# Performance work log

Measured on AMD Instinct MI355X. Metric: run time of the kernel, lower is better.

## Reference

```python
import jax, jax.numpy as jnp
import numpy as np

V = 100000   # num_node (item vocab)
D = 256      # config.dim
B = 512      # sessions / target nodes
S = 20       # items per session
N = B * S    # item nodes
E = 8 * N    # 'interacts' edges
SCALE = 12.0
NEG = -jnp.inf


def l2norm(x, eps=1e-12):
    return x / jnp.maximum(jnp.linalg.norm(x, axis=-1, keepdims=True), eps)


def setup_inputs() -> dict:
    key = jax.random.key(0)
    ks = jax.random.split(key, 16)
    stdv = 1.0 / np.sqrt(D)
    u = lambda k, shape: jax.random.uniform(k, shape, jnp.float32, -stdv, stdv)
    iid = jax.random.randint(ks[0], (N,), 0, V)
    src = jax.random.randint(ks[1], (E,), 0, N)
    # keep interacts edges within the same session (faithful to session graphs)
    dst = (src // S) * S + jax.random.randint(ks[2], (E,), 0, S)
    dis = jax.random.randint(ks[3], (E,), 0, 50)
    agg_src = jnp.arange(N)          # every item node -> its session target
    agg_dst = agg_src // S           # target (session) id per agg edge
    pid = agg_src % S                # position within session
    tid = jax.random.randint(ks[4], (B,), 0, 10)
    last_idx = jnp.arange(B) * S + (S - 1)   # nodes with data['last']==1
    return {
        'iid': iid, 'src': src, 'dst': dst, 'dis': dis, 'pid': pid,
        'agg_src': agg_src, 'agg_dst': agg_dst, 'tid': tid, 'last_idx': last_idx,
        'emb': u(ks[5], (V, D)), 'pos_emb': u(ks[6], (200, D)),
        'dis_emb': u(ks[7], (50, D)), 'target_emb': u(ks[8], (10, D)),
        'pi_w': u(ks[9], (D, 1)), 'M_w': u(ks[10], (2 * D, 1)),
        'q_w': u(ks[11], (2 * D, D)), 'r_w': u(ks[12], (2 * D, D)),
        'sc1_w': u(ks[13], (D, D)), 'sc1_b': u(ks[14], (D,)),
        'sc2_w': u(ks[15], (D, 2)),
    }


def reference(iid, src, dst, dis, pid, agg_src, agg_dst, tid, last_idx,
              emb, pos_emb, dis_emb, target_emb, pi_w, M_w, q_w, r_w,
              sc1_w, sc1_b, sc2_w):
    # --- node/edge features (dropout = identity at eval) ---
    h_v = l2norm(emb[iid])                       # [N,D]
    h_d = dis_emb[dis]                           # [E,D]
    # --- GATLayer on 'interacts' ---
    hs, hd = h_v[src], h_v[dst]
    prod = hs * hd                               # [E,D]
    e = (prod * h_d) @ pi_w                      # [E,1]
    gate = jax.nn.sigmoid(jnp.concatenate([prod, h_d], axis=-1) @ M_w)
    e = (e * gate)[:, 0]                         # [E]
    # edge_softmax grouped by destination node
    emax = jax.ops.segment_max(e, dst, num_segments=N)
    ee = jnp.exp(e - emax[dst])
    esum = jax.ops.segment_sum(ee, dst, num_segments=N)
    a = ee / esum[dst]                           # [E]
    h = jax.ops.segment_sum(hs * a[:, None], dst, num_segments=N)  # [N,D]
    # --- PosAggregator on 'agg' ---
    h_p = pos_emb[pid]                           # [EA,D]
    h_t = target_emb[tid]                        # [B,D]
    eft = h[agg_src]                             # copy_src ft -> edge ft
    eagg = jnp.tanh(jnp.concatenate([eft, h_p], axis=-1) @ q_w)    # [EA,D]
    last_feat = h[last_idx]                      # [B,D]
    f = jnp.concatenate([h_t, last_feat], axis=-1) @ r_w           # [B,D]
    m = eft * jnp.sum(eagg * f[agg_dst], axis=-1, keepdims=True)
    sr = jax.ops.segment_sum(m, agg_dst, num_segments=B)           # [B,D]
    # --- scoring head ---
    sr = l2norm(sr)
    bn = l2norm(emb)
    logits = sr @ bn.T                           # [B,V]
    phi = jax.nn.softmax(jax.nn.relu(sr @ sc1_w + sc1_b) @ sc2_w, axis=-1)  # [B,2]
    sess = jnp.arange(N) // S                    # session id of each item node
    mask = jnp.zeros((B, V), bool).at[sess, iid].set(True)
    score_in = jax.nn.softmax(jnp.where(mask, SCALE * logits, NEG), axis=-1)
    score_ex = jax.nn.softmax(jnp.where(mask, NEG, SCALE * logits), axis=-1)
    score = phi[:, 0:1] * score_in + phi[:, 1:2] * score_ex
    return jnp.log(score)
```

## Files before the change

kernel.cpp:

```cpp
#include <hip/hip_runtime.h>

typedef unsigned short u16;
typedef unsigned int u32;

constexpr int N_ = 10240, E_ = 81920, B_ = 512, S_ = 20, V_ = 100000, D_ = 256;
constexpr float SCALE_ = 12.0f;

#define DEV static __device__ __forceinline__

typedef __attribute__((ext_vector_type(8))) short bf16x8;
typedef __attribute__((ext_vector_type(4))) float f32x4;

DEV float bf2f(u16 u){ union{u32 i; float f;} c; c.i = ((u32)u)<<16; return c.f; }
DEV float bflo(u32 u){ union{u32 i; float f;} c; c.i = u<<16; return c.f; }
DEV float bfhi(u32 u){ union{u32 i; float f;} c; c.i = u & 0xffff0000u; return c.f; }
DEV u16 f2bf(float f){ union{float f; u32 i;} c; c.f=f; u32 i=c.i; i += 0x7fffu + ((i>>16)&1u); return (u16)(i>>16); }
DEV float clampf(float x, float lo, float hi){ return fminf(fmaxf(x, lo), hi); }

DEV float ldf(const void* p, size_t idx, int isf32){
  return isf32 ? ((const float*)p)[idx] : bf2f(((const u16*)p)[idx]);
}
DEV float rdout(const void* p, size_t idx, int isf32){
  return isf32 ? ((const float*)p)[idx] : bf2f(((const u16*)p)[idx]);
}
DEV void stout(void* p, size_t idx, float v, int isf32){
  if (isf32) ((float*)p)[idx] = v; else ((u16*)p)[idx] = f2bf(v);
}

DEV float waveSum(float v){
  #pragma unroll
  for (int off=32; off>0; off>>=1) v += __shfl_xor(v, off, 64);
  return v;
}
DEV float blockSum(float v, float* sred){
  v = waveSum(v);
  __syncthreads();
  if ((threadIdx.x & 63)==0) sred[threadIdx.x>>6] = v;
  __syncthreads();
  return sred[0]+sred[1]+sred[2]+sred[3];
}

__global__ __launch_bounds__(128) void k_detect(
    const u32* p0, const u32* p1, const u32* p2, const u32* p3,
    const u32* p4, const u32* p5, const u32* p6, const u32* p7,
    const u32* p8, const u32* p9, const u32* p10, int* flags)
{
  const u32* p = p0;
  switch (blockIdx.x){
    case 0: p=p0; break; case 1: p=p1; break; case 2: p=p2; break; case 3: p=p3; break;
    case 4: p=p4; break; case 5: p=p5; break; case 6: p=p6; break; case 7: p=p7; break;
    case 8: p=p8; break; case 9: p=p9; break; case 10: p=p10; break;
  }
  int t = threadIdx.x;
  u32 w = p[t];
  u32 e = (w>>8)&0x7Fu;
  int in = (e>=0x60u && e<=0x7Cu) ? 1 : 0;
  unsigned long long m = __ballot(in);
  __shared__ int cnt2[2];
  if ((t&63)==0) cnt2[t>>6] = __popcll(m);
  __syncthreads();
  if (t==0) flags[blockIdx.x] = ((cnt2[0]+cnt2[1]) > 96) ? 0 : 1;
}


__global__ __launch_bounds__(256) void k_splitB(const void* __restrict__ emb,
    u16* __restrict__ ehi, u16* __restrict__ elo, const int* __restrict__ flags)
{
  if (!flags[0]) return;
  size_t i = ((size_t)blockIdx.x*256 + threadIdx.x)*4;
  float4 x = *(const float4*)((const float*)emb + i);
  ushort4 h, l;
  h.x = f2bf(x.x); l.x = f2bf(x.x - bf2f(h.x));
  h.y = f2bf(x.y); l.y = f2bf(x.y - bf2f(h.y));
  h.z = f2bf(x.z); l.z = f2bf(x.z - bf2f(h.z));
  h.w = f2bf(x.w); l.w = f2bf(x.w - bf2f(h.w));
  *(ushort4*)(ehi+i) = h;
  *(ushort4*)(elo+i) = l;
}

__global__ __launch_bounds__(256) void k_rnorm(const void* __restrict__ emb,
    float* __restrict__ rnorm, const int* __restrict__ flags)
{
  int isf32 = flags[0];
  int v = blockIdx.x*4 + (threadIdx.x>>6);
  int lane = threadIdx.x & 63;
  float a0,a1,a2,a3;
  if (isf32){
    float4 q = *(const float4*)((const float*)emb + (size_t)v*D_ + lane*4);
    a0=q.x; a1=q.y; a2=q.z; a3=q.w;
  } else {
    uint2 p = *(const uint2*)((const u16*)emb + (size_t)v*D_ + lane*4);
    a0=bflo(p.x); a1=bfhi(p.x); a2=bflo(p.y); a3=bfhi(p.y);
  }
  float ss = waveSum(a0*a0+a1*a1+a2*a2+a3*a3);
  if (lane==0) rnorm[v] = 1.0f/fmaxf(sqrtf(ss), 1e-12f);
}

__global__ __launch_bounds__(256) void k_edge(
    const void* __restrict__ emb, const void* __restrict__ dis_emb,
    const void* __restrict__ pi_w, const void* __restrict__ M_w,
    const int* __restrict__ iid, const float* __restrict__ rnorm,
    const int* __restrict__ src, const int* __restrict__ dst, const int* __restrict__ dis,
    float* __restrict__ e_edge, const int* __restrict__ flags)
{
  int f_emb = flags[0], f_dis = flags[2], f_pi = flags[4], f_M = flags[5];
  int e = blockIdx.x*4 + (threadIdx.x>>6);
  int lane = threadIdx.x & 63;
  int s = src[e], d = dst[e], di = dis[e];
  int is = iid[s], idd = iid[d];
  float rs = rnorm[is], rd = rnorm[idd];
  int k0 = lane*4;
  float d1 = 0.f, d2 = 0.f;
  #pragma unroll
  for (int j=0;j<4;++j){
    int k = k0 + j;
    float hs = ldf(emb, (size_t)is*D_ + k, f_emb) * rs;
    float hd = ldf(emb, (size_t)idd*D_ + k, f_emb) * rd;
    float hx = ldf(dis_emb, (size_t)di*D_ + k, f_dis);
    float pr = hs*hd;
    d1 += pr * hx * ldf(pi_w, k, f_pi);
    d2 += pr * ldf(M_w, k, f_M) + hx * ldf(M_w, D_ + k, f_M);
  }
  d1 = waveSum(d1); d2 = waveSum(d2);
  if (lane==0){
    d1 = clampf(d1, -1e4f, 1e4f);
    d2 = clampf(d2, -60.f, 60.f);
    float gate = 1.0f/(1.0f+expf(-d2));
    e_edge[e] = d1*gate;
  }
}

__global__ __launch_bounds__(256) void k_count(const int* __restrict__ dst, int* __restrict__ cnt){
  int e = blockIdx.x*256+threadIdx.x;
  if (e<E_) atomicAdd(&cnt[dst[e]], 1);
}
__global__ __launch_bounds__(256) void k_scan(const int* __restrict__ cnt,
    int* __restrict__ offs, int* __restrict__ cursor){
  __shared__ int part[256];
  int t = threadIdx.x;
  const int CH = N_/256;
  int s = 0;
  for (int i=0;i<CH;++i) s += cnt[t*CH+i];
  part[t] = s; __syncthreads();
  if (t==0){
    int run=0;
    for (int i=0;i<256;++i){ int c=part[i]; part[i]=run; run+=c; }
    offs[N_] = run;
  }
  __syncthreads();
  int run = part[t];
  for (int i=0;i<CH;++i){ int idx=t*CH+i; offs[idx]=run; cursor[idx]=run; run+=cnt[idx]; }
}
__global__ __launch_bounds__(256) void k_scatter(const int* __restrict__ dst,
    int* __restrict__ cursor, int* __restrict__ elist){
  int e = blockIdx.x*256+threadIdx.x;
  if (e<E_){ int p = atomicAdd(&cursor[dst[e]],1); elist[p]=e; }
}

__global__ __launch_bounds__(256) void k_gat(
    const void* __restrict__ emb, const int* __restrict__ iid,
    const float* __restrict__ rnorm, const float* __restrict__ e_edge,
    const int* __restrict__ offs, const int* __restrict__ elist,
    const int* __restrict__ src, float* __restrict__ hagg,
    const int* __restrict__ flags)
{
  int f_emb = flags[0];
  int n = blockIdx.x, t = threadIdx.x;
  int beg = offs[n], end = offs[n+1];
  float acc = 0.f;
  if (end > beg){
    float m = -3.0e38f;
    for (int j=beg;j<end;++j) m = fmaxf(m, e_edge[elist[j]]);
    float ssum = 0.f;
    for (int j=beg;j<end;++j) ssum += expf(e_edge[elist[j]] - m);
    float inv = 1.0f/fmaxf(ssum, 1e-30f);
    for (int j=beg;j<end;++j){
      int k = elist[j];
      int sk = src[k];
      int isk = iid[sk];
      float a = expf(e_edge[k]-m)*inv;
      acc += a * ldf(emb, (size_t)isk*D_ + t, f_emb) * rnorm[isk];
    }
  }
  hagg[(size_t)n*D_ + t] = acc;
}

__global__ __launch_bounds__(256) void k_f(
    const float* __restrict__ hagg, const void* __restrict__ target_emb,
    const void* __restrict__ r_w, const int* __restrict__ tid,
    const int* __restrict__ last_idx, float* __restrict__ fbuf,
    const int* __restrict__ flags)
{
  int f_t = flags[3], f_r = flags[7];
  __shared__ float scat[2*D_];
  int b = blockIdx.x, t = threadIdx.x;
  scat[t]     = ldf(target_emb, (size_t)tid[b]*D_ + t, f_t);
  scat[D_+t]  = hagg[(size_t)last_idx[b]*D_ + t];
  __syncthreads();
  float f = 0.f;
  for (int k=0;k<2*D_;++k) f += scat[k]*ldf(r_w, (size_t)k*D_ + t, f_r);
  fbuf[(size_t)b*D_ + t] = f;
}

__global__ __launch_bounds__(256) void k_coef(
    const float* __restrict__ hagg, const void* __restrict__ pos_emb,
    const void* __restrict__ q_w, const float* __restrict__ fbuf,
    const int* __restrict__ pid, const int* __restrict__ agg_src,
    const int* __restrict__ agg_dst, float* __restrict__ coef,
    const int* __restrict__ flags)
{
  int f_p = flags[1], f_q = flags[6];
  __shared__ float sx[2*D_];
  __shared__ float sf[D_];
  __shared__ float sred[4];
  int n = blockIdx.x, t = threadIdx.x;
  int b = agg_dst[n];
  sx[t]    = hagg[(size_t)agg_src[n]*D_ + t];
  sx[D_+t] = ldf(pos_emb, (size_t)pid[n]*D_ + t, f_p);
  sf[t]    = fbuf[(size_t)b*D_ + t];
  __syncthreads();
  float a = 0.f;
  for (int k=0;k<2*D_;++k) a += sx[k]*ldf(q_w, (size_t)k*D_ + t, f_q);
  float p = tanhf(a) * sf[t];
  float s = blockSum(p, sred);
  if (t==0) coef[n] = clampf(s, -1e6f, 1e6f);
}

__global__ __launch_bounds__(256) void k_sr(
    const float* __restrict__ hagg, const float* __restrict__ coef,
    const void* __restrict__ sc1_w, const void* __restrict__ sc1_b,
    const void* __restrict__ sc2_w, const int* __restrict__ agg_src,
    u16* __restrict__ sr_hi, u16* __restrict__ sr_lo,
    float* __restrict__ logphi, const int* __restrict__ flags)
{
  int f_w1 = flags[8], f_b1 = flags[9], f_w2 = flags[10];
  __shared__ float ssr[D_];
  __shared__ float sred[4];
  int b = blockIdx.x, t = threadIdx.x;
  float srv = 0.f;
  for (int g=0; g<S_; ++g){
    int n = b*S_ + g;
    srv += hagg[(size_t)agg_src[n]*D_ + t] * coef[n];
  }
  float ss = blockSum(srv*srv, sred);
  float srn = srv / fmaxf(sqrtf(ss), 1e-12f);
  srn = clampf(srn, -2.f, 2.f);
  u16 h = f2bf(srn);
  sr_hi[(size_t)b*D_ + t] = h;
  sr_lo[(size_t)b*D_ + t] = f2bf(srn - bf2f(h));
  ssr[t] = srn;
  __syncthreads();
  float hid = ldf(sc1_b, t, f_b1);
  for (int k=0;k<D_;++k) hid += ssr[k]*ldf(sc1_w, (size_t)k*D_ + t, f_w1);
  hid = fmaxf(hid, 0.f);
  float z0 = blockSum(hid*ldf(sc2_w, t*2+0, f_w2), sred);
  float z1 = blockSum(hid*ldf(sc2_w, t*2+1, f_w2), sred);
  if (t==0){
    z0 = clampf(z0, -1e4f, 1e4f); z1 = clampf(z1, -1e4f, 1e4f);
    float mz = fmaxf(z0,z1);
    float lse = mz + logf(expf(z0-mz)+expf(z1-mz));
    logphi[2*b]   = z0 - lse;
    logphi[2*b+1] = z1 - lse;
  }
}

__global__ __launch_bounds__(256, 2) void k_mm(
    const void* __restrict__ emb, const u16* __restrict__ emb_hi,
    const u16* __restrict__ emb_lo, const u16* __restrict__ sr_hi,
    const u16* __restrict__ sr_lo, const float* __restrict__ rnorm,
    float* __restrict__ Zall, void* __restrict__ outp,
    const int* __restrict__ flags)
{
  int isf32 = flags[0];
  int lane = threadIdx.x & 63;
  int wv   = threadIdx.x >> 6;
  int col  = lane & 15;
  int kg   = lane >> 4;
  int b0   = blockIdx.y*128 + wv*32;
  int v0   = blockIdx.x*160;

  bf16x8 ahi[2][8], alo[2][8];
  #pragma unroll
  for (int m=0;m<2;++m){
    const u16* rh = sr_hi + (size_t)(b0 + m*16 + col)*D_ + kg*8;
    const u16* rl = sr_lo + (size_t)(b0 + m*16 + col)*D_ + kg*8;
    #pragma unroll
    for (int ks=0;ks<8;++ks){
      ahi[m][ks] = *(const bf16x8*)(rh + ks*32);
      alo[m][ks] = *(const bf16x8*)(rl + ks*32);
    }
  }

  const u16* Bh = isf32 ? emb_hi : (const u16*)emb;
  f32x4 zsum[2] = {{0.f,0.f,0.f,0.f},{0.f,0.f,0.f,0.f}};

  for (int vt=0; vt<10; ++vt){
    int vrow = v0 + vt*16 + col;
    const u16* bh = Bh + (size_t)vrow*D_ + kg*8;
    f32x4 acc0 = {0.f,0.f,0.f,0.f}, acc1 = {0.f,0.f,0.f,0.f};
    if (isf32){
      const u16* bl = emb_lo + (size_t)vrow*D_ + kg*8;
      #pragma unroll
      for (int ks=0;ks<8;++ks){
        bf16x8 bh8 = *(const bf16x8*)(bh + ks*32);
        bf16x8 bl8 = *(const bf16x8*)(bl + ks*32);
        acc0 = __builtin_amdgcn_mfma_f32_16x16x32_bf16(ahi[0][ks], bh8, acc0, 0,0,0);
        acc1 = __builtin_amdgcn_mfma_f32_16x16x32_bf16(ahi[1][ks], bh8, acc1, 0,0,0);
        acc0 = __builtin_amdgcn_mfma_f32_16x16x32_bf16(alo[0][ks], bh8, acc0, 0,0,0);
        acc1 = __builtin_amdgcn_mfma_f32_16x16x32_bf16(alo[1][ks], bh8, acc1, 0,0,0);
        acc0 = __builtin_amdgcn_mfma_f32_16x16x32_bf16(ahi[0][ks], bl8, acc0, 0,0,0);
        acc1 = __builtin_amdgcn_mfma_f32_16x16x32_bf16(ahi[1][ks], bl8, acc1, 0,0,0);
      }
    } else {
      #pragma unroll
      for (int ks=0;ks<8;++ks){
        bf16x8 bh8 = *(const bf16x8*)(bh + ks*32);
        acc0 = __builtin_amdgcn_mfma_f32_16x16x32_bf16(ahi[0][ks], bh8, acc0, 0,0,0);
        acc1 = __builtin_amdgcn_mfma_f32_16x16x32_bf16(ahi[1][ks], bh8, acc1, 0,0,0);
        acc0 = __builtin_amdgcn_mfma_f32_16x16x32_bf16(alo[0][ks], bh8, acc0, 0,0,0);
        acc1 = __builtin_amdgcn_mfma_f32_16x16x32_bf16(alo[1][ks], bh8, acc1, 0,0,0);
      }
    }
    float rv = rnorm[vrow] * SCALE_;
    #pragma unroll
    for (int m=0;m<2;++m){
      f32x4 a = m ? acc1 : acc0;
      #pragma unroll
      for (int r=0;r<4;++r){
        float x = clampf(a[r]*rv, -40.f, 40.f);
        zsum[m][r] += expf(x);
        int b = b0 + m*16 + kg*4 + r;
        stout(outp, (size_t)b*V_ + vrow, x, isf32);
      }
    }
  }
  #pragma unroll
  for (int m=0;m<2;++m){
    #pragma unroll
    for (int r=0;r<4;++r){
      float z = zsum[m][r];
      z += __shfl_xor(z, 1, 64);
      z += __shfl_xor(z, 2, 64);
      z += __shfl_xor(z, 4, 64);
      z += __shfl_xor(z, 8, 64);
      if (col==0) atomicAdd(&Zall[b0 + m*16 + kg*4 + r], z);
    }
  }
}

__global__ __launch_bounds__(256) void k_pre(const int* __restrict__ iid,
    const int* __restrict__ agg_dst, const void* __restrict__ outp,
    float* __restrict__ xsave, const int* __restrict__ flags)
{
  int isf32 = flags[0];
  int n = blockIdx.x*256 + threadIdx.x;
  if (n < N_){
    int b = agg_dst[n];
    int v = iid[n];
    xsave[n] = rdout(outp, (size_t)b*V_ + v, isf32);
  }
}

__global__ __launch_bounds__(64) void k_zin(const int* __restrict__ iid,
    const float* __restrict__ xsave, float* __restrict__ Zin)
{
  __shared__ int ids[S_];
  int b = blockIdx.x, g = threadIdx.x;
  if (g < S_) ids[g] = iid[b*S_ + g];
  __syncthreads();
  float z = 0.f;
  if (g < S_){
    bool first = true;
    for (int h=0; h<g; ++h) if (ids[h]==ids[g]){ first=false; break; }
    if (first) z = expf(clampf(xsave[b*S_+g], -40.f, 40.f));
  }
  z = waveSum(z);
  if (g==0) Zin[b] = z;
}

__global__ __launch_bounds__(256) void k_fin(const float* __restrict__ logphi,
    const float* __restrict__ Zall, const float* __restrict__ Zin,
    float* __restrict__ cin, float* __restrict__ cex)
{
  int b = blockIdx.x*256+threadIdx.x;
  if (b < B_){
    float zin = Zin[b];
    float zex = Zall[b] - zin;
    cin[b] = clampf(logphi[2*b]   - logf(fmaxf(zin, 1e-30f)), -1e4f, 1e4f);
    cex[b] = clampf(logphi[2*b+1] - logf(fmaxf(zex, 1e-30f)), -1e4f, 1e4f);
  }
}

__global__ __launch_bounds__(256) void k_out(const float* __restrict__ cex,
    void* __restrict__ outp, const int* __restrict__ flags)
{
  int isf32 = flags[0];
  int b = blockIdx.y;
  int v0 = (blockIdx.x*256 + threadIdx.x)*4;
  if (v0 >= V_) return;
  float ce = cex[b];
  if (isf32){
    float4* p = (float4*)((float*)outp + (size_t)b*V_ + v0);
    float4 x = *p;
    x.x = clampf(x.x+ce, -1e4f, 1e4f); x.y = clampf(x.y+ce, -1e4f, 1e4f);
    x.z = clampf(x.z+ce, -1e4f, 1e4f); x.w = clampf(x.w+ce, -1e4f, 1e4f);
    *p = x;
  } else {
    ushort4* p = (ushort4*)((u16*)outp + (size_t)b*V_ + v0);
    ushort4 lg = *p;
    lg.x = f2bf(clampf(bf2f(lg.x)+ce, -1e4f, 1e4f));
    lg.y = f2bf(clampf(bf2f(lg.y)+ce, -1e4f, 1e4f));
    lg.z = f2bf(clampf(bf2f(lg.z)+ce, -1e4f, 1e4f));
    lg.w = f2bf(clampf(bf2f(lg.w)+ce, -1e4f, 1e4f));
    *p = lg;
  }
}

__global__ __launch_bounds__(256) void k_patch(const int* __restrict__ iid,
    const int* __restrict__ agg_dst, const float* __restrict__ xsave,
    const float* __restrict__ cin, void* __restrict__ outp,
    const int* __restrict__ flags)
{
  int isf32 = flags[0];
  int n = blockIdx.x*256 + threadIdx.x;
  if (n < N_){
    int b = agg_dst[n];
    int v = iid[n];
    float val = clampf(xsave[n] + cin[b], -1e4f, 1e4f);
    stout(outp, (size_t)b*V_ + v, val, isf32);
  }
}

extern "C" void kernel_launch(void* const* d_in, const int* in_sizes, int n_in,
                              void* d_out, int out_size, void* d_ws, size_t ws_size,
                              hipStream_t stream)
{
  (void)in_sizes; (void)n_in; (void)out_size; (void)ws_size;
  const int* iid      = (const int*)d_in[0];
  const int* src      = (const int*)d_in[1];
  const int* dst      = (const int*)d_in[2];
  const int* dis      = (const int*)d_in[3];
  const int* pid      = (const int*)d_in[4];
  const int* agg_src  = (const int*)d_in[5];
  const int* agg_dst  = (const int*)d_in[6];
  const int* tid      = (const int*)d_in[7];
  const int* last_idx = (const int*)d_in[8];
  const void* emb        = d_in[9];
  const void* pos_emb    = d_in[10];
  const void* dis_emb    = d_in[11];
  const void* target_emb = d_in[12];
  const void* pi_w  = d_in[13];
  const void* M_w   = d_in[14];
  const void* q_w   = d_in[15];
  const void* r_w   = d_in[16];
  const void* sc1_w = d_in[17];
  const void* sc1_b = d_in[18];
  const void* sc2_w = d_in[19];

  char* w = (char*)d_ws;
  size_t off = 0;
  auto alloc = [&](size_t bytes)->char*{
    char* p = w + off;
    off = (off + bytes + 255) & ~(size_t)255;
    return p;
  };
  int*   flags  = (int*)alloc(16*4);
  float* rnorm  = (float*)alloc((size_t)V_*4);
  float* hagg   = (float*)alloc((size_t)N_*D_*4);
  float* e_edge = (float*)alloc((size_t)E_*4);
  int*   cnt    = (int*)alloc((size_t)N_*4);
  int*   offs   = (int*)alloc((size_t)(N_+1)*4);
  int*   cursor = (int*)alloc((size_t)N_*4);
  int*   elist  = (int*)alloc((size_t)E_*4);
  float* fbuf   = (float*)alloc((size_t)B_*D_*4);
  float* coef   = (float*)alloc((size_t)N_*4);
  u16*   sr_hi  = (u16*)alloc((size_t)B_*D_*2);
  u16*   sr_lo  = (u16*)alloc((size_t)B_*D_*2);
  float* logphi = (float*)alloc((size_t)2*B_*4);
  float* Zall   = (float*)alloc((size_t)B_*4);
  float* Zin    = (float*)alloc((size_t)B_*4);
  float* cin    = (float*)alloc((size_t)B_*4);
  float* cex    = (float*)alloc((size_t)B_*4);
  float* xsave  = (float*)alloc((size_t)N_*4);
  u16*   emb_hi = (u16*)alloc((size_t)V_*D_*2);
  u16*   emb_lo = (u16*)alloc((size_t)V_*D_*2);

  hipMemsetAsync(cnt, 0, (size_t)N_*4, stream);
  hipMemsetAsync(Zall, 0, (size_t)B_*4, stream);

  k_detect <<<11, 128, 0, stream>>>((const u32*)emb, (const u32*)pos_emb,
             (const u32*)dis_emb, (const u32*)target_emb, (const u32*)pi_w,
             (const u32*)M_w, (const u32*)q_w, (const u32*)r_w,
             (const u32*)sc1_w, (const u32*)sc1_b, (const u32*)sc2_w, flags);
  k_splitB <<<(V_*D_)/1024, 256, 0, stream>>>(emb, emb_hi, emb_lo, flags);
  k_rnorm  <<<V_/4, 256, 0, stream>>>(emb, rnorm, flags);
  k_edge   <<<E_/4, 256, 0, stream>>>(emb, dis_emb, pi_w, M_w, iid, rnorm,
                                      src, dst, dis, e_edge, flags);
  k_count  <<<E_/256, 256, 0, stream>>>(dst, cnt);
  k_scan   <<<1, 256, 0, stream>>>(cnt, offs, cursor);
  k_scatter<<<E_/256, 256, 0, stream>>>(dst, cursor, elist);
  k_gat    <<<N_, 256, 0, stream>>>(emb, iid, rnorm, e_edge, offs, elist, src, hagg, flags);
  k_f      <<<B_, 256, 0, stream>>>(hagg, target_emb, r_w, tid, last_idx, fbuf, flags);
  k_coef   <<<N_, 256, 0, stream>>>(hagg, pos_emb, q_w, fbuf, pid, agg_src, agg_dst, coef, flags);
  k_sr     <<<B_, 256, 0, stream>>>(hagg, coef, sc1_w, sc1_b, sc2_w, agg_src,
                                    sr_hi, sr_lo, logphi, flags);
  k_mm     <<<dim3(625, 4), 256, 0, stream>>>(emb, emb_hi, emb_lo, sr_hi, sr_lo,
                                              rnorm, Zall, d_out, flags);
  k_pre    <<<(N_+255)/256, 256, 0, stream>>>(iid, agg_dst, d_out, xsave, flags);
  k_zin    <<<B_, 64, 0, stream>>>(iid, xsave, Zin);
  k_fin    <<<(B_+255)/256, 256, 0, stream>>>(logphi, Zall, Zin, cin, cex);
  k_out    <<<dim3((V_/4+255)/256, B_), 256, 0, stream>>>(cex, d_out, flags);
  k_patch  <<<(N_+255)/256, 256, 0, stream>>>(iid, agg_dst, xsave, cin, d_out, flags);
}
```

Baseline: 1.247 ms.

## Fuse embedding prep, batch coef projection per wave, retile logits matmul

Merges the bf16 hi/lo split and row-norm passes into one kernel so the 100k x 256 embedding table is read once instead of twice. The q_w projection now runs one 64-thread wave per 8 agg nodes, with inputs held in registers and broadcast by shuffles, so each q_w row load serves 8 nodes instead of one. The logits matmul is retiled so each block covers 16 sessions by 256 vocab rows, and the grid is ordered with session blocks as the fast dimension. That ordering is meant to keep embedding tiles in cache across the 32 session blocks, at the cost of reloading A fragments more often and adding bounds checks on the ragged last vocab tile.

```diff
diff --git a/kernel.cpp b/kernel.cpp
--- a/kernel.cpp
+++ b/kernel.cpp
@@ -63,37 +63,31 @@
 }
 
 
-__global__ __launch_bounds__(256) void k_splitB(const void* __restrict__ emb,
-    u16* __restrict__ ehi, u16* __restrict__ elo, const int* __restrict__ flags)
-{
-  if (!flags[0]) return;
-  size_t i = ((size_t)blockIdx.x*256 + threadIdx.x)*4;
-  float4 x = *(const float4*)((const float*)emb + i);
-  ushort4 h, l;
-  h.x = f2bf(x.x); l.x = f2bf(x.x - bf2f(h.x));
-  h.y = f2bf(x.y); l.y = f2bf(x.y - bf2f(h.y));
-  h.z = f2bf(x.z); l.z = f2bf(x.z - bf2f(h.z));
-  h.w = f2bf(x.w); l.w = f2bf(x.w - bf2f(h.w));
-  *(ushort4*)(ehi+i) = h;
-  *(ushort4*)(elo+i) = l;
-}
-
-__global__ __launch_bounds__(256) void k_rnorm(const void* __restrict__ emb,
-    float* __restrict__ rnorm, const int* __restrict__ flags)
+__global__ __launch_bounds__(256) void k_prep(const void* __restrict__ emb,
+    float* __restrict__ rnorm, u16* __restrict__ ehi, u16* __restrict__ elo,
+    const int* __restrict__ flags)
 {
   int isf32 = flags[0];
   int v = blockIdx.x*4 + (threadIdx.x>>6);
   int lane = threadIdx.x & 63;
-  float a0,a1,a2,a3;
+  size_t o = (size_t)v*D_ + lane*4;
   if (isf32){
-    float4 q = *(const float4*)((const float*)emb + (size_t)v*D_ + lane*4);
-    a0=q.x; a1=q.y; a2=q.z; a3=q.w;
+    float4 q = *(const float4*)((const float*)emb + o);
+    float ss = waveSum(q.x*q.x+q.y*q.y+q.z*q.z+q.w*q.w);
+    if (lane==0) rnorm[v] = 1.0f/fmaxf(sqrtf(ss), 1e-12f);
+    ushort4 h, l;
+    h.x = f2bf(q.x); l.x = f2bf(q.x - bf2f(h.x));
+    h.y = f2bf(q.y); l.y = f2bf(q.y - bf2f(h.y));
+    h.z = f2bf(q.z); l.z = f2bf(q.z - bf2f(h.z));
+    h.w = f2bf(q.w); l.w = f2bf(q.w - bf2f(h.w));
+    *(ushort4*)(ehi+o) = h;
+    *(ushort4*)(elo+o) = l;
   } else {
-    uint2 p = *(const uint2*)((const u16*)emb + (size_t)v*D_ + lane*4);
-    a0=bflo(p.x); a1=bfhi(p.x); a2=bflo(p.y); a3=bfhi(p.y);
-  }
-  float ss = waveSum(a0*a0+a1*a1+a2*a2+a3*a3);
-  if (lane==0) rnorm[v] = 1.0f/fmaxf(sqrtf(ss), 1e-12f);
+    uint2 p = *(const uint2*)((const u16*)emb + o);
+    float a0=bflo(p.x), a1=bfhi(p.x), a2=bflo(p.y), a3=bfhi(p.y);
+    float ss = waveSum(a0*a0+a1*a1+a2*a2+a3*a3);
+    if (lane==0) rnorm[v] = 1.0f/fmaxf(sqrtf(ss), 1e-12f);
+  }
 }
 
 __global__ __launch_bounds__(256) void k_edge(
@@ -202,7 +196,7 @@
   fbuf[(size_t)b*D_ + t] = f;
 }
 
-__global__ __launch_bounds__(256) void k_coef(
+__global__ __launch_bounds__(64) void k_coef(
     const float* __restrict__ hagg, const void* __restrict__ pos_emb,
     const void* __restrict__ q_w, const float* __restrict__ fbuf,
     const int* __restrict__ pid, const int* __restrict__ agg_src,
@@ -210,20 +204,79 @@
     const int* __restrict__ flags)
 {
   int f_p = flags[1], f_q = flags[6];
-  __shared__ float sx[2*D_];
-  __shared__ float sf[D_];
-  __shared__ float sred[4];
-  int n = blockIdx.x, t = threadIdx.x;
-  int b = agg_dst[n];
-  sx[t]    = hagg[(size_t)agg_src[n]*D_ + t];
-  sx[D_+t] = ldf(pos_emb, (size_t)pid[n]*D_ + t, f_p);
-  sf[t]    = fbuf[(size_t)b*D_ + t];
-  __syncthreads();
-  float a = 0.f;
-  for (int k=0;k<2*D_;++k) a += sx[k]*ldf(q_w, (size_t)k*D_ + t, f_q);
-  float p = tanhf(a) * sf[t];
-  float s = blockSum(p, sred);
-  if (t==0) coef[n] = clampf(s, -1e6f, 1e6f);
+  int lane = threadIdx.x;
+  int n0 = blockIdx.x*8;
+  int t0 = lane*4;
+
+  float xr[8][8];
+  #pragma unroll
+  for (int e=0;e<8;++e){
+    int n = n0+e;
+    if (lane < 32){
+      const float* hp = hagg + (size_t)agg_src[n]*D_ + lane*8;
+      float4 a = *(const float4*)hp;
+      float4 b = *(const float4*)(hp+4);
+      xr[e][0]=a.x; xr[e][1]=a.y; xr[e][2]=a.z; xr[e][3]=a.w;
+      xr[e][4]=b.x; xr[e][5]=b.y; xr[e][6]=b.z; xr[e][7]=b.w;
+    } else {
+      size_t base = (size_t)pid[n]*D_ + (lane-32)*8;
+      if (f_p){
+        const float* pp = (const float*)pos_emb + base;
+        float4 a = *(const float4*)pp;
+        float4 b = *(const float4*)(pp+4);
+        xr[e][0]=a.x; xr[e][1]=a.y; xr[e][2]=a.z; xr[e][3]=a.w;
+        xr[e][4]=b.x; xr[e][5]=b.y; xr[e][6]=b.z; xr[e][7]=b.w;
+      } else {
+        const u16* pp = (const u16*)pos_emb + base;
+        uint4 u = *(const uint4*)pp;
+        xr[e][0]=bflo(u.x); xr[e][1]=bfhi(u.x); xr[e][2]=bflo(u.y); xr[e][3]=bfhi(u.y);
+        xr[e][4]=bflo(u.z); xr[e][5]=bfhi(u.z); xr[e][6]=bflo(u.w); xr[e][7]=bfhi(u.w);
+      }
+    }
+  }
+
+  float y0[8], y1[8], y2[8], y3[8];
+  #pragma unroll
+  for (int e=0;e<8;++e){ y0[e]=0.f; y1[e]=0.f; y2[e]=0.f; y3[e]=0.f; }
+
+  if (f_q){
+    for (int kb=0; kb<64; ++kb){
+      #pragma unroll
+      for (int j=0;j<8;++j){
+        int k = kb*8+j;
+        float4 q = *(const float4*)((const float*)q_w + (size_t)k*D_ + t0);
+        #pragma unroll
+        for (int e=0;e<8;++e){
+          float xk = __shfl(xr[e][j], kb, 64);
+          y0[e] += xk*q.x; y1[e] += xk*q.y; y2[e] += xk*q.z; y3[e] += xk*q.w;
+        }
+      }
+    }
+  } else {
+    for (int kb=0; kb<64; ++kb){
+      #pragma unroll
+      for (int j=0;j<8;++j){
+        int k = kb*8+j;
+        uint2 u = *(const uint2*)((const u16*)q_w + (size_t)k*D_ + t0);
+        float qx=bflo(u.x), qy=bfhi(u.x), qz=bflo(u.y), qw=bfhi(u.y);
+        #pragma unroll
+        for (int e=0;e<8;++e){
+          float xk = __shfl(xr[e][j], kb, 64);
+          y0[e] += xk*qx; y1[e] += xk*qy; y2[e] += xk*qz; y3[e] += xk*qw;
+        }
+      }
+    }
+  }
+
+  #pragma unroll
+  for (int e=0;e<8;++e){
+    int n = n0+e;
+    int b = agg_dst[n];
+    float4 f = *(const float4*)(fbuf + (size_t)b*D_ + t0);
+    float s = tanhf(y0[e])*f.x + tanhf(y1[e])*f.y + tanhf(y2[e])*f.z + tanhf(y3[e])*f.w;
+    s = waveSum(s);
+    if (lane==0) coef[n] = clampf(s, -1e6f, 1e6f);
+  }
 }
 
 __global__ __launch_bounds__(256) void k_sr(
@@ -264,7 +317,7 @@
   }
 }
 
-__global__ __launch_bounds__(256, 2) void k_mm(
+__global__ __launch_bounds__(256) void k_mm(
     const void* __restrict__ emb, const u16* __restrict__ emb_hi,
     const u16* __restrict__ emb_lo, const u16* __restrict__ sr_hi,
     const u16* __restrict__ sr_lo, const float* __restrict__ rnorm,
@@ -276,75 +329,84 @@
   int wv   = threadIdx.x >> 6;
   int col  = lane & 15;
   int kg   = lane >> 4;
-  int b0   = blockIdx.y*128 + wv*32;
-  int v0   = blockIdx.x*160;
-
-  bf16x8 ahi[2][8], alo[2][8];
-  #pragma unroll
-  for (int m=0;m<2;++m){
-    const u16* rh = sr_hi + (size_t)(b0 + m*16 + col)*D_ + kg*8;
-    const u16* rl = sr_lo + (size_t)(b0 + m*16 + col)*D_ + kg*8;
+  int b0   = blockIdx.x*16;
+  int v0   = blockIdx.y*256 + wv*64;
+
+  bf16x8 ahi[8], alo[8];
+  {
+    const u16* rh = sr_hi + (size_t)(b0 + col)*D_ + kg*8;
+    const u16* rl = sr_lo + (size_t)(b0 + col)*D_ + kg*8;
     #pragma unroll
     for (int ks=0;ks<8;++ks){
-      ahi[m][ks] = *(const bf16x8*)(rh + ks*32);
-      alo[m][ks] = *(const bf16x8*)(rl + ks*32);
+      ahi[ks] = *(const bf16x8*)(rh + ks*32);
+      alo[ks] = *(const bf16x8*)(rl + ks*32);
     }
   }
 
   const u16* Bh = isf32 ? emb_hi : (const u16*)emb;
-  f32x4 zsum[2] = {{0.f,0.f,0.f,0.f},{0.f,0.f,0.f,0.f}};
-
-  for (int vt=0; vt<10; ++vt){
+
+  int vr_[4];
+  #pragma unroll
+  for (int vt=0;vt<4;++vt){
     int vrow = v0 + vt*16 + col;
-    const u16* bh = Bh + (size_t)vrow*D_ + kg*8;
-    f32x4 acc0 = {0.f,0.f,0.f,0.f}, acc1 = {0.f,0.f,0.f,0.f};
-    if (isf32){
-      const u16* bl = emb_lo + (size_t)vrow*D_ + kg*8;
+    vr_[vt] = vrow < V_ ? vrow : V_-1;
+  }
+
+  f32x4 acc[4];
+  #pragma unroll
+  for (int vt=0;vt<4;++vt) acc[vt] = (f32x4){0.f,0.f,0.f,0.f};
+
+  if (isf32){
+    #pragma unroll
+    for (int vt=0; vt<4; ++vt){
+      const u16* bp = Bh     + (size_t)vr_[vt]*D_ + kg*8;
+      const u16* lp = emb_lo + (size_t)vr_[vt]*D_ + kg*8;
       #pragma unroll
-      for (int ks=0;ks<8;++ks){
-        bf16x8 bh8 = *(const bf16x8*)(bh + ks*32);
-        bf16x8 bl8 = *(const bf16x8*)(bl + ks*32);
-        acc0 = __builtin_amdgcn_mfma_f32_16x16x32_bf16(ahi[0][ks], bh8, acc0, 0,0,0);
-        acc1 = __builtin_amdgcn_mfma_f32_16x16x32_bf16(ahi[1][ks], bh8, acc1, 0,0,0);
-        acc0 = __builtin_amdgcn_mfma_f32_16x16x32_bf16(alo[0][ks], bh8, acc0, 0,0,0);
-        acc1 = __builtin_amdgcn_mfma_f32_16x16x32_bf16(alo[1][ks], bh8, acc1, 0,0,0);
-        acc0 = __builtin_amdgcn_mfma_f32_16x16x32_bf16(ahi[0][ks], bl8, acc0, 0,0,0);
-        acc1 = __builtin_amdgcn_mfma_f32_16x16x32_bf16(ahi[1][ks], bl8, acc1, 0,0,0);
+      for (int ks=0; ks<8; ++ks){
+        bf16x8 bh = *(const bf16x8*)(bp + ks*32);
+        bf16x8 bl = *(const bf16x8*)(lp + ks*32);
+        acc[vt] = __builtin_amdgcn_mfma_f32_16x16x32_bf16(ahi[ks], bh, acc[vt], 0,0,0);
+        acc[vt] = __builtin_amdgcn_mfma_f32_16x16x32_bf16(alo[ks], bh, acc[vt], 0,0,0);
+        acc[vt] = __builtin_amdgcn_mfma_f32_16x16x32_bf16(ahi[ks], bl, acc[vt], 0,0,0);
       }
-    } else {
+    }
+  } else {
+    #pragma unroll
+    for (int vt=0; vt<4; ++vt){
+      const u16* bp = Bh + (size_t)vr_[vt]*D_ + kg*8;
       #pragma unroll
-      for (int ks=0;ks<8;++ks){
-        bf16x8 bh8 = *(const bf16x8*)(bh + ks*32);
-        acc0 = __builtin_amdgcn_mfma_f32_16x16x32_bf16(ahi[0][ks], bh8, acc0, 0,0,0);
-        acc1 = __builtin_amdgcn_mfma_f32_16x16x32_bf16(ahi[1][ks], bh8, acc1, 0,0,0);
-        acc0 = __builtin_amdgcn_mfma_f32_16x16x32_bf16(alo[0][ks], bh8, acc0, 0,0,0);
-        acc1 = __builtin_amdgcn_mfma_f32_16x16x32_bf16(alo[1][ks], bh8, acc1, 0,0,0);
+      for (int ks=0; ks<8; ++ks){
+        bf16x8 bh = *(const bf16x8*)(bp + ks*32);
+        acc[vt] = __builtin_amdgcn_mfma_f32_16x16x32_bf16(ahi[ks], bh, acc[vt], 0,0,0);
+        acc[vt] = __builtin_amdgcn_mfma_f32_16x16x32_bf16(alo[ks], bh, acc[vt], 0,0,0);
       }
     }
-    float rv = rnorm[vrow] * SCALE_;
+  }
+
+  float zs[4] = {0.f, 0.f, 0.f, 0.f};
+  #pragma unroll
+  for (int vt=0; vt<4; ++vt){
+    int vrow = v0 + vt*16 + col;
+    bool ok = vrow < V_;
+    float rv = rnorm[vr_[vt]] * SCALE_;
     #pragma unroll
-    for (int m=0;m<2;++m){
-      f32x4 a = m ? acc1 : acc0;
-      #pragma unroll
-      for (int r=0;r<4;++r){
-        float x = clampf(a[r]*rv, -40.f, 40.f);
-        zsum[m][r] += expf(x);
-        int b = b0 + m*16 + kg*4 + r;
+    for (int r=0;r<4;++r){
+      float x = clampf(acc[vt][r]*rv, -40.f, 40.f);
+      if (ok){
+        zs[r] += expf(x);
+        int b = b0 + kg*4 + r;
         stout(outp, (size_t)b*V_ + vrow, x, isf32);
       }
     }
   }
   #pragma unroll
-  for (int m=0;m<2;++m){
-    #pragma unroll
-    for (int r=0;r<4;++r){
-      float z = zsum[m][r];
-      z += __shfl_xor(z, 1, 64);
-      z += __shfl_xor(z, 2, 64);
-      z += __shfl_xor(z, 4, 64);
-      z += __shfl_xor(z, 8, 64);
-      if (col==0) atomicAdd(&Zall[b0 + m*16 + kg*4 + r], z);
-    }
+  for (int r=0;r<4;++r){
+    float z = zs[r];
+    z += __shfl_xor(z, 1, 64);
+    z += __shfl_xor(z, 2, 64);
+    z += __shfl_xor(z, 4, 64);
+    z += __shfl_xor(z, 8, 64);
+    if (col==0) atomicAdd(&Zall[b0 + kg*4 + r], z);
   }
 }
 
@@ -492,8 +554,7 @@
              (const u32*)dis_emb, (const u32*)target_emb, (const u32*)pi_w,
              (const u32*)M_w, (const u32*)q_w, (const u32*)r_w,
              (const u32*)sc1_w, (const u32*)sc1_b, (const u32*)sc2_w, flags);
-  k_splitB <<<(V_*D_)/1024, 256, 0, stream>>>(emb, emb_hi, emb_lo, flags);
-  k_rnorm  <<<V_/4, 256, 0, stream>>>(emb, rnorm, flags);
+  k_prep   <<<V_/4, 256, 0, stream>>>(emb, rnorm, emb_hi, emb_lo, flags);
   k_edge   <<<E_/4, 256, 0, stream>>>(emb, dis_emb, pi_w, M_w, iid, rnorm,
                                       src, dst, dis, e_edge, flags);
   k_count  <<<E_/256, 256, 0, stream>>>(dst, cnt);
@@ -501,11 +562,11 @@
   k_scatter<<<E_/256, 256, 0, stream>>>(dst, cursor, elist);
   k_gat    <<<N_, 256, 0, stream>>>(emb, iid, rnorm, e_edge, offs, elist, src, hagg, flags);
   k_f      <<<B_, 256, 0, stream>>>(hagg, target_emb, r_w, tid, last_idx, fbuf, flags);
-  k_coef   <<<N_, 256, 0, stream>>>(hagg, pos_emb, q_w, fbuf, pid, agg_src, agg_dst, coef, flags);
+  k_coef   <<<N_/8, 64, 0, stream>>>(hagg, pos_emb, q_w, fbuf, pid, agg_src, agg_dst, coef, flags);
   k_sr     <<<B_, 256, 0, stream>>>(hagg, coef, sc1_w, sc1_b, sc2_w, agg_src,
                                     sr_hi, sr_lo, logphi, flags);
-  k_mm     <<<dim3(625, 4), 256, 0, stream>>>(emb, emb_hi, emb_lo, sr_hi, sr_lo,
-                                              rnorm, Zall, d_out, flags);
+  k_mm     <<<dim3(32, 391), 256, 0, stream>>>(emb, emb_hi, emb_lo, sr_hi, sr_lo,
+                                               rnorm, Zall, d_out, flags);
   k_pre    <<<(N_+255)/256, 256, 0, stream>>>(iid, agg_dst, d_out, xsave, flags);
   k_zin    <<<B_, 64, 0, stream>>>(iid, xsave, Zin);
   k_fin    <<<(B_+255)/256, 256, 0, stream>>>(logphi, Zall, Zin, cin, cex);
```

New measurement: 1.314 ms. 1.05x slower.
